# Kernel optimization log

Hardware: AMD Instinct MI355X
Metric: run time of the kernel (lower is better)

Reference implementation:

```python
import jax, jax.numpy as jnp
import numpy as np

N_NODES = 100000
N_EDGES = 1600000
IN_CH = 128
HEADS = 4
HEAD_DIM = 16  # out_channels // heads = 64 // 4
EPS = 1e-8
NEG_SLOPE = 0.2


def setup_inputs() -> dict:
    key = jax.random.key(0)
    k1, k2, k3, k4, k5 = jax.random.split(key, 5)
    x = jax.random.normal(k1, (N_NODES, IN_CH), dtype=jnp.float32)
    edge_index = jax.random.randint(k2, (2, N_EDGES), 0, N_NODES, dtype=jnp.int64)
    edge_weight = jax.random.uniform(k3, (N_EDGES,), dtype=jnp.float32)
    # Linear(in_channels, heads*head_dim, bias=False): weight [out, in]
    W = jax.random.normal(k4, (HEADS * HEAD_DIM, IN_CH), dtype=jnp.float32) * 0.05
    a = jax.random.normal(k5, (1, HEADS, 2 * HEAD_DIM), dtype=jnp.float32) * 0.1
    return {"x": x, "edge_index": edge_index, "edge_weight": edge_weight, "W": W, "a": a}


def reference(x, edge_index, edge_weight, W, a):
    num_nodes = x.shape[0]
    h = (x @ W.T).reshape(num_nodes, HEADS, HEAD_DIM)  # [N, H, D]
    src, dst = edge_index[0], edge_index[1]
    h_src = h[src]  # [E, H, D]
    h_dst = h[dst]  # [E, H, D]
    # a * concat(h_src, h_dst) summed over last dim == split-dot (avoids concat)
    a_src = a[..., :HEAD_DIM]  # [1, H, D]
    a_dst = a[..., HEAD_DIM:]  # [1, H, D]
    attention = jnp.sum(a_src * h_src + a_dst * h_dst, axis=-1)  # [E, H]
    attention = jax.nn.leaky_relu(attention, negative_slope=NEG_SLOPE)
    attention = attention * edge_weight[:, None]
    attention = jnp.exp(attention)
    att_sum = jax.ops.segment_sum(attention, dst, num_segments=num_nodes)  # [N, H]
    attention = attention / (att_sum[dst] + EPS)  # [E, H]
    # dropout is identity in eval mode
    weighted = h_src * attention[:, :, None]  # [E, H, D]
    out = jax.ops.segment_sum(weighted, dst, num_segments=num_nodes)  # [N, H, D]
    return out.reshape(num_nodes, HEADS * HEAD_DIM)
```

## Files before the change

### kernel.cpp

```cpp
#include <hip/hip_runtime.h>
#include <math.h>

#define N_NODES 100000
#define N_EDGES 1600000
#define IN_CH 128
#define HEADS 4
#define HEAD_DIM 16
#define OUT_CH 64
#define NEG_SLOPE 0.2f
#define EPS 1e-8f

#define NBUCK 391
#define NBLK1 512
#define CHUNK (N_EDGES / NBLK1)
#define CAPG 4608
#define CAP CAPG

typedef _Float16 f16x8 __attribute__((ext_vector_type(8)));
typedef _Float16 f16x4 __attribute__((ext_vector_type(4)));
typedef float    f32x4 __attribute__((ext_vector_type(4)));

__global__ __launch_bounds__(128) void prep16_kernel(
    const float* __restrict__ W, const float* __restrict__ a,
    _Float16* __restrict__ Wh)
{
    int k = threadIdx.x;
#pragma unroll
    for (int r = 0; r < 64; r++)
        Wh[r * IN_CH + k] = (_Float16)W[r * IN_CH + k];
#pragma unroll
    for (int hd = 0; hd < 4; hd++) {
        float ss = 0.f, dd = 0.f;
#pragma unroll
        for (int c = 0; c < 16; c++) {
            float wv = W[(hd * 16 + c) * IN_CH + k];
            ss += a[hd * 32 + c] * wv;
            dd += a[hd * 32 + 16 + c] * wv;
        }
        Wh[(64 + hd) * IN_CH + k] = (_Float16)ss;
        Wh[(68 + hd) * IN_CH + k] = (_Float16)dd;
    }
}

__device__ inline f16x8 cvt8(const float* p) {
    float4 lo = ((const float4*)p)[0];
    float4 hi = ((const float4*)p)[1];
    f16x8 f;
    f[0] = (_Float16)lo.x; f[1] = (_Float16)lo.y;
    f[2] = (_Float16)lo.z; f[3] = (_Float16)lo.w;
    f[4] = (_Float16)hi.x; f[5] = (_Float16)hi.y;
    f[6] = (_Float16)hi.z; f[7] = (_Float16)hi.w;
    return f;
}

__global__ __launch_bounds__(256) void gemm_alpha_kernel(
    const float* __restrict__ x,
    const _Float16* __restrict__ Wh,
    _Float16* __restrict__ h,
    float* __restrict__ alpha_src,
    float* __restrict__ alpha_dst)
{
    __shared__ _Float16 hst[128 * 72];

    const int wv = threadIdx.x >> 6;
    const int lane = threadIdx.x & 63;
    const int col = lane & 15;
    const int quad = lane >> 4;
    const int node_base = blockIdx.x * 128 + wv * 32;

    f16x8 bfrag[5][4];
#pragma unroll
    for (int nt = 0; nt < 4; nt++) {
        const _Float16* src = Wh + (nt * 16 + col) * IN_CH;
#pragma unroll
        for (int ks = 0; ks < 4; ks++)
            bfrag[nt][ks] = *(const f16x8*)(src + ks * 32 + quad * 8);
    }
    {
        const _Float16* src = Wh + (64 + (col < 8 ? col : 0)) * IN_CH;
#pragma unroll
        for (int ks = 0; ks < 4; ks++) {
            f16x8 f = *(const f16x8*)(src + ks * 32 + quad * 8);
            if (col >= 8) {
                f16x8 z = {};
                f = z;
            }
            bfrag[4][ks] = f;
        }
    }

#pragma unroll
    for (int mt = 0; mt < 2; mt++) {
        int row_node = node_base + mt * 16 + col;
        int rn = row_node < N_NODES ? row_node : N_NODES - 1;
        const float* xrow = x + (long long)rn * IN_CH;

        f16x8 afrag[4];
#pragma unroll
        for (int ks = 0; ks < 4; ks++)
            afrag[ks] = cvt8(xrow + ks * 32 + quad * 8);

        f32x4 acc[5];
#pragma unroll
        for (int nt = 0; nt < 5; nt++) {
            f32x4 z = {0.f, 0.f, 0.f, 0.f};
            acc[nt] = z;
        }
#pragma unroll
        for (int ks = 0; ks < 4; ks++)
#pragma unroll
            for (int nt = 0; nt < 5; nt++)
                acc[nt] = __builtin_amdgcn_mfma_f32_16x16x32_f16(
                    afrag[ks], bfrag[nt][ks], acc[nt], 0, 0, 0);

#pragma unroll
        for (int r = 0; r < 4; r++) {
            int nl = wv * 32 + mt * 16 + quad * 4 + r;
#pragma unroll
            for (int nt = 0; nt < 4; nt++)
                hst[nl * 72 + nt * 16 + col] = (_Float16)acc[nt][r];
            int node = node_base + mt * 16 + quad * 4 + r;
            if (node < N_NODES) {
                if (col < 4)      alpha_src[node * HEADS + col]     = acc[4][r];
                else if (col < 8) alpha_dst[node * HEADS + col - 4] = acc[4][r];
            }
        }
    }

    __syncthreads();
    const int bnode = blockIdx.x * 128;
    const int nrem = N_NODES - bnode;
    const int climit = (nrem < 128 ? nrem : 128) << 3;
    for (int i = threadIdx.x; i < 1024; i += 256) {
        if (i < climit) {
            int node = i >> 3, ch8 = i & 7;
            *(f16x8*)(h + (long long)(bnode + node) * OUT_CH + ch8 * 8) =
                *(const f16x8*)&hst[node * 72 + ch8 * 8];
        }
    }
}

__global__ __launch_bounds__(256) void fused_count_scatter_kernel(
    const int* __restrict__ ei, const float* __restrict__ ew,
    int* __restrict__ gcur,
    unsigned long long* __restrict__ tmp)
{
    __shared__ int cnt[NBUCK];
    __shared__ int dbuf[CHUNK];
    for (int j = threadIdx.x; j < NBUCK; j += 256) cnt[j] = 0;
    __syncthreads();
    const int base = blockIdx.x * CHUNK;
    for (int i = threadIdx.x; i < CHUNK; i += 256) {
        int d = ei[N_EDGES + base + i];
        dbuf[i] = d;
        atomicAdd(&cnt[d >> 8], 1);
    }
    __syncthreads();
    for (int j = threadIdx.x; j < NBUCK; j += 256) {
        int c = cnt[j];
        int b = (c > 0) ? atomicAdd(&gcur[j], c) : 0;
        cnt[j] = j * CAPG + b;
    }
    __syncthreads();
    for (int i = threadIdx.x; i < CHUNK; i += 256) {
        int e = base + i;
        int d = dbuf[i];
        int s = ei[e];
        float w = ew[e];
        int pos = atomicAdd(&cnt[d >> 8], 1);
        unsigned long long pk = ((unsigned long long)__float_as_uint(w) << 32)
                              | ((unsigned)(d & 255) << 17) | (unsigned)s;
        tmp[pos] = pk;
    }
}

__global__ __launch_bounds__(512) void bucket_offsets_kernel(
    const int* __restrict__ gcur, int* __restrict__ bucketStart,
    int* __restrict__ ptr)
{
    __shared__ int part[512];
    const int t = threadIdx.x;
    int v = (t < NBUCK) ? gcur[t] : 0;
    part[t] = v;
    __syncthreads();
    for (int off = 1; off < 512; off <<= 1) {
        int x = (t >= off) ? part[t - off] : 0;
        __syncthreads();
        part[t] += x;
        __syncthreads();
    }
    if (t < NBUCK) bucketStart[t] = part[t] - v;
    if (t == 0) { bucketStart[NBUCK] = N_EDGES; ptr[N_NODES] = N_EDGES; }
}

__global__ __launch_bounds__(256) void finalize_kernel(
    const unsigned long long* __restrict__ tmp,
    const int* __restrict__ gcur,
    const int* __restrict__ bucketStart,
    long long* __restrict__ csr, int* __restrict__ ptr)
{
    __shared__ int cnt[256];
    __shared__ int offs[256];
    __shared__ unsigned short rk[CAP];
    __shared__ unsigned long long stage[CAP];
    const int j = blockIdx.x;
    const int t = threadIdx.x;
    const int beg = bucketStart[j];
    const int len = gcur[j];
    const unsigned long long* src = tmp + (size_t)j * CAPG;

    cnt[t] = 0;
    __syncthreads();

    for (int i = t; i < len; i += 256) {
        unsigned long long pk = __builtin_nontemporal_load(&src[i]);
        stage[i] = pk;
        rk[i] = (unsigned short)atomicAdd(&cnt[(int)((pk >> 17) & 255)], 1);
    }
    __syncthreads();
    int v = cnt[t];
    for (int off = 1; off < 256; off <<= 1) {
        int x = (t >= off) ? cnt[t - off] : 0;
        __syncthreads();
        cnt[t] += x;
        __syncthreads();
    }
    int excl = cnt[t] - v;
    int node = j * 256 + t;
    if (node < N_NODES) ptr[node] = beg + excl;
    offs[t] = excl;
    __syncthreads();
    for (int i = t; i < len; i += 256) {
        unsigned long long pk = stage[i];
        int dloc = (int)((pk >> 17) & 255);
        int pos = offs[dloc] + (int)rk[i];
        unsigned long long vv = (pk & 0xFFFFFFFF00000000ull) | (pk & 0x1FFFFull);
        ((unsigned long long*)csr)[beg + pos] = vv;
    }
}

__global__ __launch_bounds__(256) void aggregate_kernel(
    const int* __restrict__ ptr,
    const int2* __restrict__ csr,
    const float4* __restrict__ alpha_src4,
    const float4* __restrict__ alpha_dst4,
    const _Float16* __restrict__ h,
    float* __restrict__ out)
{
    __shared__ float4 sev[4][64];
    __shared__ int    ssc[4][64];

    const int wv = threadIdx.x >> 6;
    const int lane = threadIdx.x & 63;
    const int n = blockIdx.x * 4 + wv;
    if (n >= N_NODES) return;
    const int q = lane >> 4;
    const int cg = lane & 15;
    const int hsel = cg >> 2;

    const int beg = ptr[n];
    const int end = ptr[n + 1];
    const float4 ad4 = alpha_dst4[n];

    float4 acc = make_float4(0.f, 0.f, 0.f, 0.f);
    float denom = 0.f;
    float4* sev_w = sev[wv];
    int* ssc_w = ssc[wv];

    for (int base = beg; base < end; base += 64) {
        int cnt = min(64, end - base);
        int s_l = 0;
        float4 e4 = make_float4(0.f, 0.f, 0.f, 0.f);
        if (lane < cnt) {
            int2 pr = csr[base + lane];
            s_l = pr.x;
            float w = __int_as_float(pr.y);
            float4 as = alpha_src4[s_l];
            float t0 = as.x + ad4.x; t0 = (t0 > 0.f ? t0 : NEG_SLOPE * t0) * w;
            float t1 = as.y + ad4.y; t1 = (t1 > 0.f ? t1 : NEG_SLOPE * t1) * w;
            float t2 = as.z + ad4.z; t2 = (t2 > 0.f ? t2 : NEG_SLOPE * t2) * w;
            float t3 = as.w + ad4.w; t3 = (t3 > 0.f ? t3 : NEG_SLOPE * t3) * w;
            e4 = make_float4(__expf(t0), __expf(t1), __expf(t2), __expf(t3));
        }
        sev_w[lane] = e4;
        ssc_w[lane] = s_l;

        int iters = (cnt + 3) >> 2;
        for (int j0 = 0; j0 < iters; j0 += 2) {
            int idx0 = j0 * 4 + q;
            int idx1 = idx0 + 4;
            int s0 = ssc_w[idx0];
            int s1 = ssc_w[idx1];
            float ev0 = ((const float*)&sev_w[idx0])[hsel];
            float ev1 = ((const float*)&sev_w[idx1])[hsel];
            f16x4 h0 = *(const f16x4*)(h + s0 * OUT_CH + cg * 4);
            f16x4 h1 = *(const f16x4*)(h + s1 * OUT_CH + cg * 4);
            acc.x += ev0 * (float)h0[0] + ev1 * (float)h1[0];
            acc.y += ev0 * (float)h0[1] + ev1 * (float)h1[1];
            acc.z += ev0 * (float)h0[2] + ev1 * (float)h1[2];
            acc.w += ev0 * (float)h0[3] + ev1 * (float)h1[3];
            denom += ev0 + ev1;
        }
    }

    denom += __shfl_xor(denom, 16);
    denom += __shfl_xor(denom, 32);
    acc.x += __shfl_xor(acc.x, 16);  acc.x += __shfl_xor(acc.x, 32);
    acc.y += __shfl_xor(acc.y, 16);  acc.y += __shfl_xor(acc.y, 32);
    acc.z += __shfl_xor(acc.z, 16);  acc.z += __shfl_xor(acc.z, 32);
    acc.w += __shfl_xor(acc.w, 16);  acc.w += __shfl_xor(acc.w, 32);

    if (lane < 16) {
        float inv = 1.f / (denom + EPS);
        float4 r = make_float4(acc.x * inv, acc.y * inv, acc.z * inv, acc.w * inv);
        ((float4*)(out + (long long)n * OUT_CH))[cg] = r;
    }
}

extern "C" void kernel_launch(void* const* d_in, const int* in_sizes, int n_in,
                              void* d_out, int out_size, void* d_ws, size_t ws_size,
                              hipStream_t stream) {
    const float* x  = (const float*)d_in[0];
    const int*   ei = (const int*)d_in[1];
    const float* ew = (const float*)d_in[2];
    const float* W  = (const float*)d_in[3];
    const float* a  = (const float*)d_in[4];
    float* out = (float*)d_out;

    char* p = (char*)d_ws;
    _Float16* h      = (_Float16*)p; p += (size_t)N_NODES * OUT_CH * 2;
    float* alpha_src = (float*)p;  p += (size_t)N_NODES * HEADS * 4;
    float* alpha_dst = (float*)p;  p += (size_t)N_NODES * HEADS * 4;
    _Float16* Wh     = (_Float16*)p; p += (size_t)72 * IN_CH * 2;
    int*   gcur      = (int*)p;    p += (size_t)392 * 4;
    int*   bstart    = (int*)p;    p += (size_t)392 * 4;
    int*   ptr       = (int*)p;    p += (size_t)(N_NODES + 4) * 4;
    unsigned long long* tmp = (unsigned long long*)p;
    p += (size_t)NBUCK * CAPG * 8;
    long long* csr   = (long long*)p;

    hipMemsetAsync(gcur, 0, 392 * sizeof(int), stream);

    prep16_kernel<<<1, 128, 0, stream>>>(W, a, Wh);
    fused_count_scatter_kernel<<<NBLK1, 256, 0, stream>>>(ei, ew, gcur, tmp);
    bucket_offsets_kernel<<<1, 512, 0, stream>>>(gcur, bstart, ptr);
    gemm_alpha_kernel<<<(N_NODES + 127) / 128, 256, 0, stream>>>(x, Wh, h, alpha_src, alpha_dst);
    finalize_kernel<<<NBUCK, 256, 0, stream>>>(tmp, gcur, bstart, csr, ptr);
    aggregate_kernel<<<(N_NODES + 3) / 4, 256, 0, stream>>>(
        ptr, (const int2*)csr, (const float4*)alpha_src, (const float4*)alpha_dst, h, out);
}
```

Before: 211.0 us.

## Stage W fragments in swizzled LDS, widen blocks to 512 threads, fold memset

```diff
diff --git a/kernel.cpp b/kernel.cpp
--- a/kernel.cpp
+++ b/kernel.cpp
@@ -20,11 +20,14 @@
 typedef _Float16 f16x4 __attribute__((ext_vector_type(4)));
 typedef float    f32x4 __attribute__((ext_vector_type(4)));
 
+#define SWZ(b) ((b) ^ ((((b) >> 8) & 7) << 4))
+
 __global__ __launch_bounds__(128) void prep16_kernel(
     const float* __restrict__ W, const float* __restrict__ a,
-    _Float16* __restrict__ Wh)
+    _Float16* __restrict__ Wh, int* __restrict__ gcur)
 {
     int k = threadIdx.x;
+    for (int i = k; i < NBUCK + 1; i += 128) gcur[i] = 0;
 #pragma unroll
     for (int r = 0; r < 64; r++)
         Wh[r * IN_CH + k] = (_Float16)W[r * IN_CH + k];
@@ -53,77 +56,70 @@
     return f;
 }
 
-__global__ __launch_bounds__(256) void gemm_alpha_kernel(
+__global__ __launch_bounds__(512, 6) void gemm_alpha_kernel(
     const float* __restrict__ x,
     const _Float16* __restrict__ Wh,
     _Float16* __restrict__ h,
     float* __restrict__ alpha_src,
     float* __restrict__ alpha_dst)
 {
+    __shared__ _Float16 whs[72 * 128];
     __shared__ _Float16 hst[128 * 72];
 
     const int wv = threadIdx.x >> 6;
     const int lane = threadIdx.x & 63;
     const int col = lane & 15;
     const int quad = lane >> 4;
-    const int node_base = blockIdx.x * 128 + wv * 32;
-
-    f16x8 bfrag[5][4];
-#pragma unroll
-    for (int nt = 0; nt < 4; nt++) {
-        const _Float16* src = Wh + (nt * 16 + col) * IN_CH;
-#pragma unroll
-        for (int ks = 0; ks < 4; ks++)
-            bfrag[nt][ks] = *(const f16x8*)(src + ks * 32 + quad * 8);
-    }
-    {
-        const _Float16* src = Wh + (64 + (col < 8 ? col : 0)) * IN_CH;
-#pragma unroll
-        for (int ks = 0; ks < 4; ks++) {
-            f16x8 f = *(const f16x8*)(src + ks * 32 + quad * 8);
-            if (col >= 8) {
+
+    for (int c = threadIdx.x; c < 1152; c += 512) {
+        int b = c << 4;
+        *(f16x8*)((char*)whs + SWZ(b)) = *(const f16x8*)((const char*)Wh + b);
+    }
+    __syncthreads();
+
+    const int node_base = blockIdx.x * 128 + wv * 16;
+    int row_node = node_base + col;
+    int rn = row_node < N_NODES ? row_node : N_NODES - 1;
+    const float* xrow = x + (long long)rn * IN_CH;
+
+    f16x8 afrag[4];
+#pragma unroll
+    for (int ks = 0; ks < 4; ks++)
+        afrag[ks] = cvt8(xrow + ks * 32 + quad * 8);
+
+    f32x4 acc[5];
+#pragma unroll
+    for (int nt = 0; nt < 5; nt++) {
+        f32x4 z = {0.f, 0.f, 0.f, 0.f};
+        acc[nt] = z;
+    }
+
+#pragma unroll
+    for (int ks = 0; ks < 4; ks++) {
+#pragma unroll
+        for (int nt = 0; nt < 5; nt++) {
+            int r = (nt < 4) ? nt * 16 + col : 64 + (col & 7);
+            int b = (r << 8) + (ks << 6) + (quad << 4);
+            f16x8 bf = *(const f16x8*)((const char*)whs + SWZ(b));
+            if (nt == 4 && col >= 8) {
                 f16x8 z = {};
-                f = z;
+                bf = z;
             }
-            bfrag[4][ks] = f;
-        }
-    }
-
-#pragma unroll
-    for (int mt = 0; mt < 2; mt++) {
-        int row_node = node_base + mt * 16 + col;
-        int rn = row_node < N_NODES ? row_node : N_NODES - 1;
-        const float* xrow = x + (long long)rn * IN_CH;
-
-        f16x8 afrag[4];
-#pragma unroll
-        for (int ks = 0; ks < 4; ks++)
-            afrag[ks] = cvt8(xrow + ks * 32 + quad * 8);
-
-        f32x4 acc[5];
-#pragma unroll
-        for (int nt = 0; nt < 5; nt++) {
-            f32x4 z = {0.f, 0.f, 0.f, 0.f};
-            acc[nt] = z;
-        }
-#pragma unroll
-        for (int ks = 0; ks < 4; ks++)
-#pragma unroll
-            for (int nt = 0; nt < 5; nt++)
-                acc[nt] = __builtin_amdgcn_mfma_f32_16x16x32_f16(
-                    afrag[ks], bfrag[nt][ks], acc[nt], 0, 0, 0);
-
-#pragma unroll
-        for (int r = 0; r < 4; r++) {
-            int nl = wv * 32 + mt * 16 + quad * 4 + r;
-#pragma unroll
-            for (int nt = 0; nt < 4; nt++)
-                hst[nl * 72 + nt * 16 + col] = (_Float16)acc[nt][r];
-            int node = node_base + mt * 16 + quad * 4 + r;
-            if (node < N_NODES) {
-                if (col < 4)      alpha_src[node * HEADS + col]     = acc[4][r];
-                else if (col < 8) alpha_dst[node * HEADS + col - 4] = acc[4][r];
-            }
+            acc[nt] = __builtin_amdgcn_mfma_f32_16x16x32_f16(
+                afrag[ks], bf, acc[nt], 0, 0, 0);
+        }
+    }
+
+#pragma unroll
+    for (int r = 0; r < 4; r++) {
+        int nl = wv * 16 + quad * 4 + r;
+#pragma unroll
+        for (int nt = 0; nt < 4; nt++)
+            hst[nl * 72 + nt * 16 + col] = (_Float16)acc[nt][r];
+        int node = node_base + quad * 4 + r;
+        if (node < N_NODES) {
+            if (col < 4)      alpha_src[node * HEADS + col]     = acc[4][r];
+            else if (col < 8) alpha_dst[node * HEADS + col - 4] = acc[4][r];
         }
     }
 
@@ -131,7 +127,7 @@
     const int bnode = blockIdx.x * 128;
     const int nrem = N_NODES - bnode;
     const int climit = (nrem < 128 ? nrem : 128) << 3;
-    for (int i = threadIdx.x; i < 1024; i += 256) {
+    for (int i = threadIdx.x; i < 1024; i += 512) {
         if (i < climit) {
             int node = i >> 3, ch8 = i & 7;
             *(f16x8*)(h + (long long)(bnode + node) * OUT_CH + ch8 * 8) =
@@ -140,29 +136,29 @@
     }
 }
 
-__global__ __launch_bounds__(256) void fused_count_scatter_kernel(
+__global__ __launch_bounds__(512) void fused_count_scatter_kernel(
     const int* __restrict__ ei, const float* __restrict__ ew,
     int* __restrict__ gcur,
     unsigned long long* __restrict__ tmp)
 {
     __shared__ int cnt[NBUCK];
     __shared__ int dbuf[CHUNK];
-    for (int j = threadIdx.x; j < NBUCK; j += 256) cnt[j] = 0;
+    for (int j = threadIdx.x; j < NBUCK; j += 512) cnt[j] = 0;
     __syncthreads();
     const int base = blockIdx.x * CHUNK;
-    for (int i = threadIdx.x; i < CHUNK; i += 256) {
+    for (int i = threadIdx.x; i < CHUNK; i += 512) {
         int d = ei[N_EDGES + base + i];
         dbuf[i] = d;
         atomicAdd(&cnt[d >> 8], 1);
     }
     __syncthreads();
-    for (int j = threadIdx.x; j < NBUCK; j += 256) {
+    for (int j = threadIdx.x; j < NBUCK; j += 512) {
         int c = cnt[j];
         int b = (c > 0) ? atomicAdd(&gcur[j], c) : 0;
         cnt[j] = j * CAPG + b;
     }
     __syncthreads();
-    for (int i = threadIdx.x; i < CHUNK; i += 256) {
+    for (int i = threadIdx.x; i < CHUNK; i += 512) {
         int e = base + i;
         int d = dbuf[i];
         int s = ei[e];
@@ -193,7 +189,7 @@
     if (t == 0) { bucketStart[NBUCK] = N_EDGES; ptr[N_NODES] = N_EDGES; }
 }
 
-__global__ __launch_bounds__(256) void finalize_kernel(
+__global__ __launch_bounds__(512) void finalize_kernel(
     const unsigned long long* __restrict__ tmp,
     const int* __restrict__ gcur,
     const int* __restrict__ bucketStart,
@@ -209,28 +205,30 @@
     const int len = gcur[j];
     const unsigned long long* src = tmp + (size_t)j * CAPG;
 
-    cnt[t] = 0;
-    __syncthreads();
-
-    for (int i = t; i < len; i += 256) {
+    if (t < 256) cnt[t] = 0;
+    __syncthreads();
+
+    for (int i = t; i < len; i += 512) {
         unsigned long long pk = __builtin_nontemporal_load(&src[i]);
         stage[i] = pk;
         rk[i] = (unsigned short)atomicAdd(&cnt[(int)((pk >> 17) & 255)], 1);
     }
     __syncthreads();
-    int v = cnt[t];
+    int v = (t < 256) ? cnt[t] : 0;
     for (int off = 1; off < 256; off <<= 1) {
-        int x = (t >= off) ? cnt[t - off] : 0;
+        int x = (t < 256 && t >= off) ? cnt[t - off] : 0;
         __syncthreads();
-        cnt[t] += x;
+        if (t < 256) cnt[t] += x;
         __syncthreads();
     }
-    int excl = cnt[t] - v;
-    int node = j * 256 + t;
-    if (node < N_NODES) ptr[node] = beg + excl;
-    offs[t] = excl;
-    __syncthreads();
-    for (int i = t; i < len; i += 256) {
+    if (t < 256) {
+        int excl = cnt[t] - v;
+        int node = j * 256 + t;
+        if (node < N_NODES) ptr[node] = beg + excl;
+        offs[t] = excl;
+    }
+    __syncthreads();
+    for (int i = t; i < len; i += 512) {
         unsigned long long pk = stage[i];
         int dloc = (int)((pk >> 17) & 255);
         int pos = offs[dloc] + (int)rk[i];
@@ -339,13 +337,11 @@
     p += (size_t)NBUCK * CAPG * 8;
     long long* csr   = (long long*)p;
 
-    hipMemsetAsync(gcur, 0, 392 * sizeof(int), stream);
-
-    prep16_kernel<<<1, 128, 0, stream>>>(W, a, Wh);
-    fused_count_scatter_kernel<<<NBLK1, 256, 0, stream>>>(ei, ew, gcur, tmp);
+    prep16_kernel<<<1, 128, 0, stream>>>(W, a, Wh, gcur);
+    fused_count_scatter_kernel<<<NBLK1, 512, 0, stream>>>(ei, ew, gcur, tmp);
     bucket_offsets_kernel<<<1, 512, 0, stream>>>(gcur, bstart, ptr);
-    gemm_alpha_kernel<<<(N_NODES + 127) / 128, 256, 0, stream>>>(x, Wh, h, alpha_src, alpha_dst);
-    finalize_kernel<<<NBUCK, 256, 0, stream>>>(tmp, gcur, bstart, csr, ptr);
+    gemm_alpha_kernel<<<(N_NODES + 127) / 128, 512, 0, stream>>>(x, Wh, h, alpha_src, alpha_dst);
+    finalize_kernel<<<NBUCK, 512, 0, stream>>>(tmp, gcur, bstart, csr, ptr);
     aggregate_kernel<<<(N_NODES + 3) / 4, 256, 0, stream>>>(
         ptr, (const int2*)csr, (const float4*)alpha_src, (const float4*)alpha_dst, h, out);
 }
```

After: 205.3 us. 2.7% less time.
